# Kernel optimization log

Hardware: AMD Instinct MI355X
Metric: run time of the kernel (lower is better)

The kernel has to match this reference:

```python
import jax, jax.numpy as jnp
import numpy as np

# --- problem sizes (fixed channel widths come from the module's irreps arithmetic) ---
N, E = 100000, 1600000
NUM_ELEM, F0, RB, HID = 4, 4, 10, 10          # len(atomic_list), embedding_dim[0], embedding_dim[1], hidden_dim
EDGE_DIM, SH_DIM = 2 * F0 + RB, 9             # 18, lmax=2 -> 1+3+5
GATE_IN, GATE_OUT = 92, 76                    # 12 scalars + 16 gates + 64 gated ; 12 + 64
CUTOFF, P_ENV, AVG_DEG = 5.0, 6, 16.0


def setup_inputs() -> dict:
    key = jax.random.key(0)
    ks = jax.random.split(key, 16)
    d = {}
    d["type_indices"] = jax.random.randint(ks[0], (N,), 0, NUM_ELEM)
    d["positions"] = jax.random.uniform(ks[1], (N, 3), dtype=jnp.float32) * 6.0
    # radius_graph replaced by a fixed-size random edge list (jit-friendly, same downstream math)
    d["edge_src"] = jax.random.randint(ks[2], (E,), 0, N)
    d["edge_dest"] = jax.random.randint(ks[3], (E,), 0, N)
    d["embed_table"] = jax.random.normal(ks[4], (NUM_ELEM, F0), dtype=jnp.float32)
    fins = [F0, GATE_OUT, GATE_OUT]
    fouts = [GATE_IN, GATE_IN, 1]
    for i in range(3):
        d[f"mlp{i+1}_w1"] = jax.random.normal(ks[5 + 3 * i], (EDGE_DIM, HID), dtype=jnp.float32) / np.float32(np.sqrt(EDGE_DIM))
        d[f"mlp{i+1}_w2"] = jax.random.normal(ks[6 + 3 * i], (HID, SH_DIM), dtype=jnp.float32) / np.float32(np.sqrt(HID))
        d[f"tp{i+1}"] = jax.random.normal(ks[7 + 3 * i], (SH_DIM, fins[i], fouts[i]), dtype=jnp.float32) / np.float32(np.sqrt(fins[i]))
    return d


def sph_harmonics(vec):
    # real spherical harmonics up to l=2, 'component' normalization, on normalized vectors
    r = jnp.linalg.norm(vec, axis=-1, keepdims=True)
    u = vec / jnp.maximum(r, 1e-9)
    x, y, z = u[:, 0], u[:, 1], u[:, 2]
    c1 = np.float32(np.sqrt(3.0))
    c2 = np.float32(np.sqrt(15.0))
    c2b = np.float32(np.sqrt(5.0) / 2.0)
    return jnp.stack([
        jnp.ones_like(x),
        c1 * y, c1 * z, c1 * x,
        c2 * x * y, c2 * y * z, c2b * (3.0 * z * z - 1.0), c2 * x * z, (c2 / 2.0) * (x * x - y * y),
    ], axis=-1)  # [E, 9]


def radial_embed(r):
    # Bessel radial basis with DimeNet-style polynomial envelope (p=6)
    x = r / CUTOFF                                    # [E, 1]
    n = jnp.arange(1, RB + 1, dtype=jnp.float32)      # [RB]
    bess = np.float32(np.sqrt(2.0 / CUTOFF)) * jnp.sin(n * jnp.pi * x) / jnp.maximum(r, 1e-9)
    p = P_ENV
    env = (1.0 - (p + 1) * (p + 2) / 2.0 * x ** p + p * (p + 2) * x ** (p + 1) - p * (p + 1) / 2.0 * x ** (p + 2))
    return bess * env                                 # [E, RB]


def gate(x):
    # e3nn Gate: scalars 4x0e(relu)+8x0o(abs), gates 4x0e(relu)+4x0o(tanh)+4x0e(relu)+4x0o(tanh),
    # gated irreps 4x1o+4x1e (3 comps each) + 4x2e+4x2o (5 comps each)
    s, g, v = x[:, :12], x[:, 12:28], x[:, 28:]
    s_act = jnp.concatenate([jax.nn.relu(s[:, :4]), jnp.abs(s[:, 4:])], axis=-1)
    g_act = jnp.concatenate([jax.nn.relu(g[:, 0:4]), jnp.tanh(g[:, 4:8]),
                             jax.nn.relu(g[:, 8:12]), jnp.tanh(g[:, 12:16])], axis=-1)
    g_exp = jnp.concatenate([jnp.repeat(g_act[:, :8], 3, axis=1),   # 8 gates x 3 comps (l=1)
                             jnp.repeat(g_act[:, 8:], 5, axis=1)],  # 8 gates x 5 comps (l=2)
                            axis=-1)                                 # [*, 64]
    return jnp.concatenate([s_act, v * g_exp], axis=-1)             # [*, 76]


def conv(x, edge_src, edge_dest, sh, edge_embed, w1, w2, tp):
    # per-edge weights from 2-layer MLP on edge embedding, one weight per SH component (factorized TP)
    w = jax.nn.relu(edge_embed @ w1) @ w2             # [E, 9]
    shw = sh * w                                      # [E, 9]
    xg = x[edge_src]                                  # gather [E, F_in]
    msg = shw[:, 0:1] * (xg @ tp[0])
    for s in range(1, SH_DIM):                        # fixed small loop over SH components
        msg = msg + shw[:, s:s + 1] * (xg @ tp[s])
    out = jax.ops.segment_sum(msg, edge_dest, num_segments=x.shape[0])
    return out / np.float32(np.sqrt(AVG_DEG))


def reference(type_indices, positions, edge_src, edge_dest, embed_table,
              mlp1_w1, mlp1_w2, tp1, mlp2_w1, mlp2_w2, tp2, mlp3_w1, mlp3_w2, tp3):
    te = embed_table[type_indices]                            # [N, 4]
    ev = positions[edge_dest] - positions[edge_src]           # [E, 3]
    el = jnp.linalg.norm(ev, axis=-1, keepdims=True)          # [E, 1]
    ee = jnp.concatenate([te[edge_dest], te[edge_src], radial_embed(el)], axis=-1)  # [E, 18]
    sh = sph_harmonics(ev)                                    # [E, 9]
    x0 = te
    x1 = gate(conv(x0, edge_src, edge_dest, sh, ee, mlp1_w1, mlp1_w2, tp1))
    x1 = x1.at[:, :F0].add(x0)                                # scalar-channel residual
    x2 = gate(conv(x1, edge_src, edge_dest, sh, ee, mlp2_w1, mlp2_w2, tp2)) + x1
    x3 = conv(x2, edge_src, edge_dest, sh, ee, mlp3_w1, mlp3_w2, tp3)  # [N, 1]
    return jnp.sum(x3)
```

## Files before the change

kernel.cpp:

```cpp
#include <hip/hip_runtime.h>
#include <hip/hip_bf16.h>
#include <math.h>

typedef unsigned int uint32;
typedef __attribute__((ext_vector_type(8))) short short8;
typedef __attribute__((ext_vector_type(4))) float f32x4;

#define TBINS 1024
#define RMAX  10.4f
#define BSHIFT 7
#define BDR    (1<<BSHIFT)

__device__ __forceinline__ uint32 pack_bf16(float a, float b){
  __hip_bfloat16 ba = __float2bfloat16(a);
  __hip_bfloat16 bb = __float2bfloat16(b);
  unsigned short ua = *reinterpret_cast<unsigned short*>(&ba);
  unsigned short ub = *reinterpret_cast<unsigned short*>(&bb);
  return (uint32)ua | ((uint32)ub << 16);
}
__device__ __forceinline__ float bf_lo(uint32 u){ return __uint_as_float(u << 16); }
__device__ __forceinline__ float bf_hi(uint32 u){ return __uint_as_float(u & 0xffff0000u); }


__global__ __launch_bounds__(1024) void k_bcount(
    const int* __restrict__ esrc, const int* __restrict__ edst,
    int* __restrict__ gb1, int* __restrict__ gb2, int E){
  __shared__ int c1[1024], c2[1024];
  int tid = threadIdx.x;
  c1[tid] = 0; c2[tid] = 0;
  __syncthreads();
  int e0 = blockIdx.x * 8192;
  #pragma unroll
  for (int k=0;k<8;k++){
    int e = e0 + k*1024 + tid;
    if (e < E){
      atomicAdd(&c1[edst[e] >> BSHIFT], 1);
      atomicAdd(&c2[esrc[e] >> BSHIFT], 1);
    }
  }
  __syncthreads();
  if (c1[tid]) atomicAdd(&gb1[tid], c1[tid]);
  if (c2[tid]) atomicAdd(&gb2[tid], c2[tid]);
}


__global__ __launch_bounds__(1024) void k_bscan(
    const int* __restrict__ gb1, const int* __restrict__ gb2,
    int* __restrict__ boff1, int* __restrict__ boff2,
    int* __restrict__ gcur1, int* __restrict__ gcur2,
    int* __restrict__ offsets, int* __restrict__ off2,
    int N, int E, int NBUCK){
  __shared__ int sm[1024];
  int tid = threadIdx.x;
  int v = (tid < NBUCK) ? gb1[tid] : 0;
  sm[tid] = v; __syncthreads();
  for (int off=1; off<1024; off<<=1){
    int t = (tid >= off) ? sm[tid-off] : 0;
    __syncthreads();
    sm[tid] += t;
    __syncthreads();
  }
  if (tid < NBUCK){ int o = sm[tid]-v; boff1[tid] = o; gcur1[tid] = o; }
  __syncthreads();
  int v2 = (tid < NBUCK) ? gb2[tid] : 0;
  sm[tid] = v2; __syncthreads();
  for (int off=1; off<1024; off<<=1){
    int t = (tid >= off) ? sm[tid-off] : 0;
    __syncthreads();
    sm[tid] += t;
    __syncthreads();
  }
  if (tid < NBUCK){ int o = sm[tid]-v2; boff2[tid] = o; gcur2[tid] = o; }
  if (tid == 0){
    boff1[NBUCK] = E; boff2[NBUCK] = E;
    offsets[N] = E;   off2[N] = E;
  }
}


__global__ __launch_bounds__(1024) void k_binA2(
    const int* __restrict__ esrc, const int* __restrict__ edst,
    int* __restrict__ gcur1, int* __restrict__ gcur2,
    int2* __restrict__ pair1, int2* __restrict__ pair2, int E, int NBUCK){
  __shared__ int cnt1[1024], run1[1024];
  __shared__ int cnt2[1024], run2[1024];
  int tid = threadIdx.x;
  int e0 = blockIdx.x * 8192;
  cnt1[tid] = 0; cnt2[tid] = 0;
  __syncthreads();
  #pragma unroll
  for (int k=0;k<8;k++){
    int e = e0 + k*1024 + tid;
    if (e < E){
      atomicAdd(&cnt1[edst[e] >> BSHIFT], 1);
      atomicAdd(&cnt2[esrc[e] >> BSHIFT], 1);
    }
  }
  __syncthreads();
  if (tid < NBUCK){
    if (cnt1[tid] > 0) run1[tid] = atomicAdd(&gcur1[tid], cnt1[tid]);
    if (cnt2[tid] > 0) run2[tid] = atomicAdd(&gcur2[tid], cnt2[tid]);
  }
  __syncthreads();
  #pragma unroll
  for (int k=0;k<8;k++){
    int e = e0 + k*1024 + tid;
    if (e < E){
      int s = esrc[e], d = edst[e];
      int p1 = atomicAdd(&run1[d >> BSHIFT], 1);
      int2 pr1; pr1.x = s; pr1.y = d;
      pair1[p1] = pr1;
      int p2 = atomicAdd(&run2[s >> BSHIFT], 1);
      int2 pr2; pr2.x = d; pr2.y = s;
      pair2[p2] = pr2;
    }
  }
}


__global__ __launch_bounds__(256) void k_binB2(
    const int2* __restrict__ pair, const int* __restrict__ boff,
    int* __restrict__ offsets, int* __restrict__ csr_out, int N){
  __shared__ int cnt[BDR];
  __shared__ int scn[BDR];
  int base = blockIdx.x << BSHIFT;
  int hi = base + BDR; if (hi > N) hi = N;
  int nloc = hi - base;
  if (nloc <= 0) return;
  int tid = threadIdx.x;
  if (tid < BDR) cnt[tid] = 0;
  __syncthreads();
  int p0 = boff[blockIdx.x], p1 = boff[blockIdx.x+1];
  for (int p = p0 + tid; p < p1; p += 256) atomicAdd(&cnt[pair[p].y - base], 1);
  __syncthreads();
  int val = (tid < BDR) ? cnt[tid] : 0;
  if (tid < BDR) scn[tid] = val;
  __syncthreads();
  for (int off=1; off<BDR; off<<=1){
    int t = (tid >= off && tid < BDR) ? scn[tid-off] : 0;
    __syncthreads();
    if (tid < BDR) scn[tid] += t;
    __syncthreads();
  }
  if (tid < nloc){
    int o = p0 + scn[tid] - val;
    offsets[base + tid] = o;
    cnt[tid] = o;
  }
  __syncthreads();
  for (int p = p0 + tid; p < p1; p += 256){
    int2 pr = pair[p];
    int slot = atomicAdd(&cnt[pr.y - base], 1);
    csr_out[slot] = pr.x;
  }
}


__global__ void k_pack(const float* __restrict__ pos, const int* __restrict__ types,
                       float4* __restrict__ ptyp, int N){
  int i = blockIdx.x*256 + threadIdx.x;
  if (i >= N) return;
  float4 f; f.x = pos[3*i]; f.y = pos[3*i+1]; f.z = pos[3*i+2]; f.w = __int_as_float(types[i]);
  ptyp[i] = f;
}


__device__ __forceinline__ void radial_mlp(
    float r, int td, int ts, const float* sEmb,
    const float* sW1, const float* sW2, float* w_out ){
  float ee[18];
  #pragma unroll
  for (int i=0;i<4;i++){ ee[i] = sEmb[td*4+i]; ee[4+i] = sEmb[ts*4+i]; }
  float rm = fmaxf(r, 1e-9f);
  float inv = 1.f/rm;
  float xx = r * 0.2f;
  float x2v = xx*xx, x3v = x2v*xx, x6 = x3v*x3v, x7 = x6*xx, x8 = x7*xx;
  float env = 1.f - 28.f*x6 + 48.f*x7 - 21.f*x8;
  const float bc = 0.6324555320336759f;
  float pref = bc * env * inv;
  const float PI = 3.14159265358979323846f;
  float s1, cth;
  __sincosf(PI*xx, &s1, &cth);
  float two_c = 2.f*cth;
  float sp = 0.f, sc = s1;
  ee[8] = pref * sc;
  #pragma unroll
  for (int n=2;n<=10;n++){
    float sn = two_c*sc - sp;
    sp = sc; sc = sn;
    ee[7+n] = pref * sc;
  }
  float h[10];
  #pragma unroll
  for (int j=0;j<10;j++){
    float a = 0.f;
    #pragma unroll
    for (int k=0;k<18;k++) a = fmaf(ee[k], sW1[k*10+j], a);
    h[j] = fmaxf(a, 0.f);
  }
  #pragma unroll
  for (int sj=0;sj<9;sj++){
    float a = 0.f;
    #pragma unroll
    for (int j=0;j<10;j++) a = fmaf(h[j], sW2[j*9+sj], a);
    w_out[sj] = a;
  }
}


__global__ __launch_bounds__(256) void k_mktab(
    const float* __restrict__ embed,
    const float* __restrict__ w1a, const float* __restrict__ w2a,
    const float* __restrict__ w1b, const float* __restrict__ w2b,
    const float* __restrict__ w1c, const float* __restrict__ w2c,
    uint32* __restrict__ tab){
  __shared__ float sEmb[16];
  __shared__ float sW1a[180], sW2a[90], sW1b[180], sW2b[90], sW1c[180], sW2c[90];
  int t = threadIdx.x;
  if (t < 16) sEmb[t] = embed[t];
  if (t < 180){ sW1a[t] = w1a[t]; sW1b[t] = w1b[t]; sW1c[t] = w1c[t]; }
  if (t < 90){  sW2a[t] = w2a[t]; sW2b[t] = w2b[t]; sW2c[t] = w2c[t]; }
  __syncthreads();
  int gid = blockIdx.x*256 + t;
  if (gid >= 16*TBINS) return;
  int combo = gid / TBINS, bin = gid - combo*TBINS;
  int td = combo >> 2, ts = combo & 3;
  const float dR = RMAX / TBINS;
  float r0 = bin*dR, r1 = r0 + dR;
  float a0[9], a1[9], b0[9], b1[9], c0[9], c1[9];
  radial_mlp(r0, td, ts, sEmb, sW1a, sW2a, a0);
  radial_mlp(r1, td, ts, sEmb, sW1a, sW2a, a1);
  radial_mlp(r0, td, ts, sEmb, sW1b, sW2b, b0);
  radial_mlp(r1, td, ts, sEmb, sW1b, sW2b, b1);
  radial_mlp(r0, td, ts, sEmb, sW1c, sW2c, c0);
  radial_mlp(r1, td, ts, sEmb, sW1c, sW2c, c1);
  uint32* rec = tab + (size_t)gid*32;
  #pragma unroll
  for (int s=0;s<9;s++){
    rec[s]    = pack_bf16(a0[s], a1[s]-a0[s]);
    rec[9+s]  = pack_bf16(b0[s], b1[s]-b0[s]);
    rec[18+s] = pack_bf16(c0[s], c1[s]-c0[s]);
  }
  #pragma unroll
  for (int s=27;s<32;s++) rec[s] = 0u;
}


__global__ __launch_bounds__(256) void k_layer12t(
    const int* __restrict__ offsets, const int* __restrict__ csr_src,
    const float4* __restrict__ ptyp, const float* __restrict__ embed,
    const uint32* __restrict__ tab, const float* __restrict__ tp1,
    float* __restrict__ x1, uint32* __restrict__ shwb, int N, int E){
  __shared__ float sT[36*92];
  __shared__ float sEmb[16];
  int t = threadIdx.x;
  if (t < 16) sEmb[t] = embed[t];
  for (int i=t; i<36*92; i+=256) sT[i] = tp1[i]*0.25f;
  __syncthreads();
  int gid = blockIdx.x*256 + t;
  int n = gid >> 2, q = gid & 3;
  if (n >= N) return;
  float4 fd = ptyp[n];
  float dx = fd.x, dy = fd.y, dz = fd.z;
  int td = __float_as_int(fd.w);
  const float c1 = 1.7320508075688772f, c2 = 3.872983346207417f, c2b = 1.118033988749895f;
  const float invD = (float)TBINS / RMAX;
  float Z[36];
  #pragma unroll
  for (int i=0;i<36;i++) Z[i]=0.f;
  int b0 = offsets[n], b1 = offsets[n+1];
  for (int j=b0+q; j<b1; j+=4){
    int s = csr_src[j];
    float4 fs = ptyp[s];
    float px = dx - fs.x, py = dy - fs.y, pz = dz - fs.z;
    int ts_ = __float_as_int(fs.w);
    float r = sqrtf(px*px + py*py + pz*pz);
    float inv = 1.f/fmaxf(r, 1e-9f);
    float ux = px*inv, uy = py*inv, uz = pz*inv;
    float sh[9];
    sh[0]=1.f; sh[1]=c1*uy; sh[2]=c1*uz; sh[3]=c1*ux;
    sh[4]=c2*ux*uy; sh[5]=c2*uy*uz; sh[6]=c2b*(3.f*uz*uz-1.f); sh[7]=c2*ux*uz;
    sh[8]=0.5f*c2*(ux*ux-uy*uy);
    float tt = r * invD;
    int bb = (int)tt; bb = (bb > TBINS-1) ? TBINS-1 : bb;
    float frac = tt - (float)bb;
    const uint32* rec = tab + ((size_t)((td*4+ts_)*TBINS + bb))*32;
    uint32 R[20];
    #pragma unroll
    for (int i=0;i<5;i++) *(uint4*)&R[i*4] = *(const uint4*)(rec + i*4);
    float x0[4];
    #pragma unroll
    for (int i=0;i<4;i++) x0[i] = sEmb[ts_*4+i];
    float sw2[9];
    #pragma unroll
    for (int sj=0;sj<9;sj++){
      uint32 ua = R[sj], ub = R[9+sj];
      float w1v = fmaf(frac, bf_hi(ua), bf_lo(ua));
      float w2v = fmaf(frac, bf_hi(ub), bf_lo(ub));
      float s1v = sh[sj]*w1v;
      sw2[sj] = sh[sj]*w2v;
      #pragma unroll
      for (int i=0;i<4;i++) Z[sj*4+i] = fmaf(s1v, x0[i], Z[sj*4+i]);
    }
    shwb[j]             = pack_bf16(sw2[0],sw2[1]);
    shwb[(size_t)E+j]   = pack_bf16(sw2[2],sw2[3]);
    shwb[(size_t)2*E+j] = pack_bf16(sw2[4],sw2[5]);
    shwb[(size_t)3*E+j] = pack_bf16(sw2[6],sw2[7]);
    shwb[(size_t)4*E+j] = pack_bf16(sw2[8],0.f);
  }
  #pragma unroll
  for (int m=1; m<=2; m<<=1){
    #pragma unroll
    for (int i=0;i<36;i++) Z[i] += __shfl_xor(Z[i], m, 4);
  }
  float* xo = x1 + (size_t)n*76;
  int gi_prev = -1; float ga = 0.f;
  for (int cc=q*19; cc<q*19+19; cc++){
    float v;
    if (cc < 12){
      float y = 0.f;
      #pragma unroll
      for (int p=0;p<36;p++) y = fmaf(Z[p], sT[p*92+cc], y);
      v = (cc<4) ? (fmaxf(y,0.f) + sEmb[td*4+cc]) : fabsf(y);
    } else {
      int j = cc - 12;
      int gi = (j<24) ? (j/3) : (8 + (j-24)/5);
      if (gi != gi_prev){
        float gy = 0.f;
        #pragma unroll
        for (int p=0;p<36;p++) gy = fmaf(Z[p], sT[p*92+12+gi], gy);
        ga = (gi<4 || (gi>=8 && gi<12)) ? fmaxf(gy,0.f) : tanhf(gy);
        gi_prev = gi;
      }
      float y = 0.f;
      #pragma unroll
      for (int p=0;p<36;p++) y = fmaf(Z[p], sT[p*92+28+j], y);
      v = y*ga;
    }
    xo[cc] = v;
  }
}


__global__ void k_cast(const float* __restrict__ x1, uint32* __restrict__ x1b, int n38){
  int i = blockIdx.x*256 + threadIdx.x;
  if (i >= n38) return;
  float2 f = *(const float2*)&x1[(size_t)i*2];
  x1b[i] = pack_bf16(f.x, f.y);
}


__global__ __launch_bounds__(256) void k_conv2c(
    const int* __restrict__ offsets, const int* __restrict__ csr_src,
    const uint32* __restrict__ shwb, const uint32* __restrict__ x1b,
    uint32* __restrict__ Z2u, int d0, int dend, int E){
  int g = blockIdx.x*256 + threadIdx.x;
  int dg = g/38;
  int u = g - dg*38;
  int d = d0 + dg;
  if (d >= dend) return;
  float z[9], zb[9];
  #pragma unroll
  for (int s=0;s<9;s++){ z[s]=0.f; zb[s]=0.f; }
  int b0 = offsets[d], b1 = offsets[d+1];
  for (int j=b0;j<b1;j++){
    int sn = csr_src[j];
    uint32 xv = x1b[(size_t)sn*38 + u];
    float xa = bf_lo(xv), xb = bf_hi(xv);
    uint32 a0 = shwb[j];
    uint32 a1 = shwb[(size_t)E+j];
    uint32 a2 = shwb[(size_t)2*E+j];
    uint32 a3 = shwb[(size_t)3*E+j];
    uint32 a4 = shwb[(size_t)4*E+j];
    float w[9];
    w[0]=bf_lo(a0); w[1]=bf_hi(a0); w[2]=bf_lo(a1); w[3]=bf_hi(a1);
    w[4]=bf_lo(a2); w[5]=bf_hi(a2); w[6]=bf_lo(a3); w[7]=bf_hi(a3); w[8]=bf_lo(a4);
    #pragma unroll
    for (int s=0;s<9;s++){
      z[s]  = fmaf(w[s], xa, z[s]);
      zb[s] = fmaf(w[s], xb, zb[s]);
    }
  }
  uint32* zr = Z2u + (size_t)dg*352;
  #pragma unroll
  for (int s=0;s<9;s++) zr[s*38+u] = pack_bf16(z[s], zb[s]);
  if (u < 10) zr[342+u] = 0u;
}


__global__ void k_wprep2(const float* __restrict__ tp2, unsigned short* __restrict__ Wt){
  int q = blockIdx.x*256 + threadIdx.x;
  if (q >= 22*96*32) return;
  int kin = q & 31;
  int rest = q >> 5;
  int col = rest % 96, s = rest / 96;
  int k = s*32 + kin;
  float v = (k < 684 && col < 92) ? tp2[k*92+col]*0.25f : 0.f;
  __hip_bfloat16 b = __float2bfloat16(v);
  Wt[q] = *reinterpret_cast<unsigned short*>(&b);
}


__global__ __launch_bounds__(256) void k_gemm2m(
    const uint32* __restrict__ Z2u, const unsigned short* __restrict__ Wt,
    const float* __restrict__ x1, const float* __restrict__ tp3,
    float* __restrict__ A, int d0, int dend){
  __shared__ float lw[64][100];
  __shared__ float tl3[684];
  int t = threadIdx.x;
  for (int i=t;i<684;i+=256) tl3[i] = tp3[i]*0.25f;
  int w = t >> 6, l = t & 63;
  int lrow = l & 15, lk = l >> 4;
  int mb = blockIdx.x*64;
  const uint32* arow = Z2u + (size_t)(mb + w*16 + lrow)*352 + lk*4;
  const short8* bb = (const short8*)Wt;
  int boff = lrow*4 + lk;
  f32x4 acc[6];
  #pragma unroll
  for (int ct=0;ct<6;ct++) acc[ct] = (f32x4){0.f,0.f,0.f,0.f};
  for (int s=0;s<22;s++){
    short8 af = *(const short8*)(arow + s*16);
    #pragma unroll
    for (int ct=0;ct<6;ct++){
      short8 bf = bb[(s*96 + ct*16)*4 + boff];
      acc[ct] = __builtin_amdgcn_mfma_f32_16x16x32_bf16(af, bf, acc[ct], 0, 0, 0);
    }
  }
  #pragma unroll
  for (int ct=0;ct<6;ct++)
    #pragma unroll
    for (int i=0;i<4;i++)
      lw[w*16 + lk*4 + i][ct*16 + lrow] = acc[ct][i];
  __syncthreads();
  int m = t>>2, q = t&3;
  int node = d0 + mb + m;
  float pA[9];
  #pragma unroll
  for (int s=0;s<9;s++) pA[s]=0.f;
  if (node < dend){
    const float* xr = x1 + (size_t)node*76;
    for (int cc=q*19; cc<q*19+19; cc++){
      float v;
      if (cc < 12){
        float y = lw[m][cc];
        v = (cc<4) ? fmaxf(y,0.f) : fabsf(y);
      } else {
        int j = cc-12;
        int gi = (j<24) ? (j/3) : (8 + (j-24)/5);
        float gy = lw[m][12+gi];
        float ga = (gi<4 || (gi>=8 && gi<12)) ? fmaxf(gy,0.f) : tanhf(gy);
        v = lw[m][28+j]*ga;
      }
      float xv = v + xr[cc];
      #pragma unroll
      for (int s=0;s<9;s++) pA[s] = fmaf(xv, tl3[s*76+cc], pA[s]);
    }
  }
  #pragma unroll
  for (int off=1; off<=2; off<<=1){
    #pragma unroll
    for (int s=0;s<9;s++) pA[s] += __shfl_xor(pA[s], off, 4);
  }
  if (node < dend && q == 0){
    float* Ar = A + (size_t)node*16;
    float4 w0 = {pA[0],pA[1],pA[2],pA[3]};
    float4 w1 = {pA[4],pA[5],pA[6],pA[7]};
    *(float4*)Ar = w0;
    *(float4*)(Ar+4) = w1;
    Ar[8] = pA[8];
  }
}


__global__ __launch_bounds__(256) void k_g3t(
    const int* __restrict__ off2, const int* __restrict__ csr2_dst,
    const float4* __restrict__ ptyp, const uint32* __restrict__ tab,
    float* __restrict__ G, int N){
  int gid = blockIdx.x*256 + threadIdx.x;
  int n = gid >> 2, q = gid & 3;
  if (n >= N) return;
  float acc[9];
  #pragma unroll
  for (int s=0;s<9;s++) acc[s]=0.f;
  float4 fs = ptyp[n];
  float sx = fs.x, sy = fs.y, sz = fs.z;
  int ts_ = __float_as_int(fs.w);
  const float c1 = 1.7320508075688772f, c2 = 3.872983346207417f, c2b = 1.118033988749895f;
  const float invD = (float)TBINS / RMAX;
  int b0 = off2[n], b1 = off2[n+1];
  for (int j=b0+q; j<b1; j+=4){
    int d = csr2_dst[j];
    float4 fdd = ptyp[d];
    float px = fdd.x-sx, py = fdd.y-sy, pz = fdd.z-sz;
    int td_ = __float_as_int(fdd.w);
    float r = sqrtf(px*px + py*py + pz*pz);
    float inv = 1.f/fmaxf(r, 1e-9f);
    float ux = px*inv, uy = py*inv, uz = pz*inv;
    float sh[9];
    sh[0]=1.f; sh[1]=c1*uy; sh[2]=c1*uz; sh[3]=c1*ux;
    sh[4]=c2*ux*uy; sh[5]=c2*uy*uz; sh[6]=c2b*(3.f*uz*uz-1.f); sh[7]=c2*ux*uz;
    sh[8]=0.5f*c2*(ux*ux-uy*uy);
    float tt = r * invD;
    int bb = (int)tt; bb = (bb > TBINS-1) ? TBINS-1 : bb;
    float frac = tt - (float)bb;
    const uint32* rec = tab + ((size_t)((td_*4+ts_)*TBINS + bb))*32;
    uint32 R[12];
    #pragma unroll
    for (int i=0;i<3;i++) *(uint4*)&R[i*4] = *(const uint4*)(rec + 16 + i*4);
    #pragma unroll
    for (int sj=0;sj<9;sj++){
      uint32 u = R[2+sj];
      float w = fmaf(frac, bf_hi(u), bf_lo(u));
      acc[sj] = fmaf(sh[sj], w, acc[sj]);
    }
  }
  #pragma unroll
  for (int off=2; off>0; off>>=1){
    #pragma unroll
    for (int s=0;s<9;s++) acc[s] += __shfl_down(acc[s], off, 4);
  }
  if (q == 0){
    float* gr = G + (size_t)n*12;
    float4 w0 = {acc[0],acc[1],acc[2],acc[3]};
    float4 w1 = {acc[4],acc[5],acc[6],acc[7]};
    *(float4*)gr = w0;
    *(float4*)(gr+4) = w1;
    gr[8] = acc[8];
  }
}


__global__ __launch_bounds__(256) void k_finalG(
    const float* __restrict__ G, const float* __restrict__ A,
    float* __restrict__ out, int N){
  int n = blockIdx.x*256 + threadIdx.x;
  float part = 0.f;
  if (n < N){
    const float* gr = G + (size_t)n*12;
    const float* Ar = A + (size_t)n*16;
    float4 g0 = *(const float4*)gr, g1 = *(const float4*)(gr+4);
    float4 a0 = *(const float4*)Ar, a1 = *(const float4*)(Ar+4);
    part = g0.x*a0.x + g0.y*a0.y + g0.z*a0.z + g0.w*a0.w
         + g1.x*a1.x + g1.y*a1.y + g1.z*a1.z + g1.w*a1.w
         + gr[8]*Ar[8];
  }
  #pragma unroll
  for (int off=32; off>0; off>>=1) part += __shfl_down(part, off, 64);
  if ((threadIdx.x & 63) == 0) atomicAdd(out, part);
}


extern "C" void kernel_launch(void* const* d_in, const int* in_sizes, int n_in,
                              void* d_out, int out_size, void* d_ws, size_t ws_size,
                              hipStream_t stream){
  const int*   types = (const int*)d_in[0];
  const float* pos   = (const float*)d_in[1];
  const int*   esrc  = (const int*)d_in[2];
  const int*   edst  = (const int*)d_in[3];
  const float* embed = (const float*)d_in[4];
  const float* m1w1=(const float*)d_in[5],  *m1w2=(const float*)d_in[6],  *tp1=(const float*)d_in[7];
  const float* m2w1=(const float*)d_in[8],  *m2w2=(const float*)d_in[9],  *tp2=(const float*)d_in[10];
  const float* m3w1=(const float*)d_in[11], *m3w2=(const float*)d_in[12], *tp3=(const float*)d_in[13];
  int N = in_sizes[0];
  int E = in_sizes[2];
  float* out = (float*)d_out;

  char* wsb = (char*)d_ws; size_t off = 0;
  auto alloc = [&](size_t b)->char*{ char* p = wsb + off; off = (off + b + 255) & ~(size_t)255; return p; };
  float*  x1      = (float*)alloc((size_t)N*76*sizeof(float));
  uint32* x1b     = (uint32*)alloc((size_t)N*38*sizeof(uint32));
  float4* ptyp    = (float4*)alloc((size_t)N*sizeof(float4));
  uint32* shwb    = (uint32*)alloc((size_t)E*5*sizeof(uint32));
  int*    csr_src = (int*)alloc((size_t)E*sizeof(int));
  int*    csr2_dst= (int*)alloc((size_t)E*sizeof(int));
  int2*   pair1   = (int2*)alloc((size_t)E*sizeof(int2));
  int2*   pair2   = (int2*)alloc((size_t)E*sizeof(int2));
  int*    offsets = (int*)alloc((size_t)(N+1)*sizeof(int));
  int*    off2    = (int*)alloc((size_t)(N+1)*sizeof(int));
  int*    gb1     = (int*)alloc(1024*sizeof(int));
  int*    gb2     = (int*)alloc(1024*sizeof(int));
  int*    boff1   = (int*)alloc(1025*sizeof(int));
  int*    boff2   = (int*)alloc(1025*sizeof(int));
  int*    gcur1   = (int*)alloc(1024*sizeof(int));
  int*    gcur2   = (int*)alloc(1024*sizeof(int));
  unsigned short* Wt = (unsigned short*)alloc((size_t)22*96*32*sizeof(unsigned short));
  float*  A       = (float*)alloc((size_t)N*16*sizeof(float));
  float*  G       = (float*)alloc((size_t)N*12*sizeof(float));
  uint32* tab     = (uint32*)alloc((size_t)16*TBINS*32*sizeof(uint32));

  size_t avail = (ws_size > off) ? (ws_size - off - 512) : 0;
  long long rows = (long long)(avail / (352*sizeof(uint32))) - 64;
  int CH = (rows > 50176) ? 50176 : (int)rows;
  CH = (CH / 64) * 64;
  if (CH < 64) CH = 64;
  uint32* Z2u = (uint32*)alloc((size_t)(CH+64)*352*sizeof(uint32));

  hipMemsetAsync(gb1, 0, 2048*sizeof(int), stream);
  hipMemsetAsync(out, 0, sizeof(float), stream);

  int nbN = (N+255)/256;
  int nbT = (16*TBINS+255)/256;
  int NBUCK = (N + BDR - 1) >> BSHIFT;
  int nbC = (E+8191)/8192;
  k_pack<<<nbN,256,0,stream>>>(pos, types, ptyp, N);
  k_mktab<<<nbT,256,0,stream>>>(embed, m1w1, m1w2, m2w1, m2w2, m3w1, m3w2, tab);
  k_bcount<<<nbC,1024,0,stream>>>(esrc, edst, gb1, gb2, E);
  k_bscan<<<1,1024,0,stream>>>(gb1, gb2, boff1, boff2, gcur1, gcur2,
                               offsets, off2, N, E, NBUCK);
  k_binA2<<<nbC,1024,0,stream>>>(esrc, edst, gcur1, gcur2, pair1, pair2, E, NBUCK);
  k_binB2<<<NBUCK,256,0,stream>>>(pair1, boff1, offsets, csr_src, N);
  k_binB2<<<NBUCK,256,0,stream>>>(pair2, boff2, off2, csr2_dst, N);

  k_wprep2<<<(22*96*32+255)/256,256,0,stream>>>(tp2, Wt);

  k_g3t<<<(4*N+255)/256,256,0,stream>>>(off2, csr2_dst, ptyp, tab, G, N);

  k_layer12t<<<(4*N+255)/256,256,0,stream>>>(offsets, csr_src, ptyp, embed,
                                             tab, tp1, x1, shwb, N, E);
  k_cast<<<(N*38+255)/256,256,0,stream>>>(x1, x1b, N*38);

  for (int d0 = 0; d0 < N; d0 += CH){
    int dend = (d0 + CH < N) ? (d0 + CH) : N;
    int nn = dend - d0;
    k_conv2c<<<((nn*38)+255)/256,256,0,stream>>>(offsets, csr_src, shwb, x1b, Z2u, d0, dend, E);
    k_gemm2m<<<(nn+63)/64,256,0,stream>>>(Z2u, Wt, x1, tp3, A, d0, dend);
  }

  k_finalG<<<nbN,256,0,stream>>>(G, A, out, N);
}
```

Baseline: 499.4 us.

## Parallelize layer-1 edge work over block edges with LDS atomic accumulation by source type

The layer-1 kernel previously gave each destination node four threads that walked its edges, accumulating a 36-float register array. Each block now covers 64 destination nodes and spreads their contiguous CSR edge range evenly across all 256 threads, using a binary search over local offsets to find each edge's destination. Per-edge results are folded into a per-node, per-source-type 9-wide sum in shared memory with atomics, and the embedding is applied afterwards. This is meant to fix load imbalance from variable node degree and to cut per-edge FMAs, at the cost of LDS atomic contention, the binary search, and an extra synchronization.

```diff
diff --git a/kernel.cpp b/kernel.cpp
--- a/kernel.cpp
+++ b/kernel.cpp
@@ -246,33 +246,37 @@
 }
 
 
-__global__ __launch_bounds__(256) void k_layer12t(
+__global__ __launch_bounds__(256) void k_edgeA2(
     const int* __restrict__ offsets, const int* __restrict__ csr_src,
     const float4* __restrict__ ptyp, const float* __restrict__ embed,
     const uint32* __restrict__ tab, const float* __restrict__ tp1,
     float* __restrict__ x1, uint32* __restrict__ shwb, int N, int E){
   __shared__ float sT[36*92];
   __shared__ float sEmb[16];
+  __shared__ float S[64*36];
+  __shared__ int loff[65];
   int t = threadIdx.x;
+  int n0 = blockIdx.x*64;
+  int nloc = N - n0; if (nloc > 64) nloc = 64;
+  if (nloc <= 0) return;
   if (t < 16) sEmb[t] = embed[t];
   for (int i=t; i<36*92; i+=256) sT[i] = tp1[i]*0.25f;
-  __syncthreads();
-  int gid = blockIdx.x*256 + t;
-  int n = gid >> 2, q = gid & 3;
-  if (n >= N) return;
-  float4 fd = ptyp[n];
-  float dx = fd.x, dy = fd.y, dz = fd.z;
-  int td = __float_as_int(fd.w);
+  for (int i=t; i<64*36; i+=256) S[i] = 0.f;
+  for (int i=t; i<=64; i+=256) loff[i] = offsets[n0 + (i<nloc ? i : nloc)];
+  __syncthreads();
   const float c1 = 1.7320508075688772f, c2 = 3.872983346207417f, c2b = 1.118033988749895f;
   const float invD = (float)TBINS / RMAX;
-  float Z[36];
-  #pragma unroll
-  for (int i=0;i<36;i++) Z[i]=0.f;
-  int b0 = offsets[n], b1 = offsets[n+1];
-  for (int j=b0+q; j<b1; j+=4){
+  int p0 = loff[0], p1 = loff[64];
+  for (int j = p0 + t; j < p1; j += 256){
+    int lo = 0, hi = 64;
+    #pragma unroll
+    for (int it=0; it<6; it++){ int mid = (lo+hi)>>1; if (loff[mid] <= j) lo = mid; else hi = mid; }
+    int d = lo;
+    float4 fd = ptyp[n0+d];
+    int td = __float_as_int(fd.w);
     int s = csr_src[j];
     float4 fs = ptyp[s];
-    float px = dx - fs.x, py = dy - fs.y, pz = dz - fs.z;
+    float px = fd.x - fs.x, py = fd.y - fs.y, pz = fd.z - fs.z;
     int ts_ = __float_as_int(fs.w);
     float r = sqrtf(px*px + py*py + pz*pz);
     float inv = 1.f/fmaxf(r, 1e-9f);
@@ -288,19 +292,15 @@
     uint32 R[20];
     #pragma unroll
     for (int i=0;i<5;i++) *(uint4*)&R[i*4] = *(const uint4*)(rec + i*4);
-    float x0[4];
-    #pragma unroll
-    for (int i=0;i<4;i++) x0[i] = sEmb[ts_*4+i];
+    float* Sd = &S[d*36 + ts_*9];
     float sw2[9];
     #pragma unroll
     for (int sj=0;sj<9;sj++){
       uint32 ua = R[sj], ub = R[9+sj];
       float w1v = fmaf(frac, bf_hi(ua), bf_lo(ua));
       float w2v = fmaf(frac, bf_hi(ub), bf_lo(ub));
-      float s1v = sh[sj]*w1v;
       sw2[sj] = sh[sj]*w2v;
-      #pragma unroll
-      for (int i=0;i<4;i++) Z[sj*4+i] = fmaf(s1v, x0[i], Z[sj*4+i]);
+      atomicAdd(&Sd[sj], sh[sj]*w1v);
     }
     shwb[j]             = pack_bf16(sw2[0],sw2[1]);
     shwb[(size_t)E+j]   = pack_bf16(sw2[2],sw2[3]);
@@ -308,11 +308,22 @@
     shwb[(size_t)3*E+j] = pack_bf16(sw2[6],sw2[7]);
     shwb[(size_t)4*E+j] = pack_bf16(sw2[8],0.f);
   }
-  #pragma unroll
-  for (int m=1; m<=2; m<<=1){
-    #pragma unroll
-    for (int i=0;i<36;i++) Z[i] += __shfl_xor(Z[i], m, 4);
-  }
+  __syncthreads();
+  int d = t >> 2, q = t & 3;
+  if (d >= nloc) return;
+  int n = n0 + d;
+  int td = __float_as_int(ptyp[n].w);
+  float Z[36];
+  const float* Sd = &S[d*36];
+  #pragma unroll
+  for (int sj=0;sj<9;sj++)
+    #pragma unroll
+    for (int i=0;i<4;i++){
+      float z = 0.f;
+      #pragma unroll
+      for (int t4=0;t4<4;t4++) z = fmaf(sEmb[t4*4+i], Sd[t4*9+sj], z);
+      Z[sj*4+i] = z;
+    }
   float* xo = x1 + (size_t)n*76;
   int gi_prev = -1; float ga = 0.f;
   for (int cc=q*19; cc<q*19+19; cc++){
@@ -599,6 +610,7 @@
   hipMemsetAsync(out, 0, sizeof(float), stream);
 
   int nbN = (N+255)/256;
+  int nbB = (N+63)/64;
   int nbT = (16*TBINS+255)/256;
   int NBUCK = (N + BDR - 1) >> BSHIFT;
   int nbC = (E+8191)/8192;
@@ -615,8 +627,8 @@
 
   k_g3t<<<(4*N+255)/256,256,0,stream>>>(off2, csr2_dst, ptyp, tab, G, N);
 
-  k_layer12t<<<(4*N+255)/256,256,0,stream>>>(offsets, csr_src, ptyp, embed,
-                                             tab, tp1, x1, shwb, N, E);
+  k_edgeA2<<<nbB,256,0,stream>>>(offsets, csr_src, ptyp, embed, tab, tp1,
+                                 x1, shwb, N, E);
   k_cast<<<(N*38+255)/256,256,0,stream>>>(x1, x1b, N*38);
 
   for (int d0 = 0; d0 < N; d0 += CH){
```

Result: slower. 554.6 us (+11.1%).

## Fuse layer-2 edge aggregation and MFMA GEMM into one kernel via LDS

Applied to the files above, without the earlier changes.

Merges the chunked conv2 aggregation kernel and the MFMA GEMM/gate kernel into one kernel. Each block now aggregates 32 destination nodes into an LDS tile and runs the bf16 MFMA GEMM from LDS instead of from a global Z2 buffer. This removes the global write and re-read of the large intermediate and the chunked launch loop. In exchange, blocks are smaller, use more LDS, and leave half the threads idle in the epilogue. The per-block gather phase can also be imbalanced across nodes of different degree.

```diff
diff --git a/kernel.cpp b/kernel.cpp
--- a/kernel.cpp
+++ b/kernel.cpp
@@ -350,44 +350,6 @@
 }
 
 
-__global__ __launch_bounds__(256) void k_conv2c(
-    const int* __restrict__ offsets, const int* __restrict__ csr_src,
-    const uint32* __restrict__ shwb, const uint32* __restrict__ x1b,
-    uint32* __restrict__ Z2u, int d0, int dend, int E){
-  int g = blockIdx.x*256 + threadIdx.x;
-  int dg = g/38;
-  int u = g - dg*38;
-  int d = d0 + dg;
-  if (d >= dend) return;
-  float z[9], zb[9];
-  #pragma unroll
-  for (int s=0;s<9;s++){ z[s]=0.f; zb[s]=0.f; }
-  int b0 = offsets[d], b1 = offsets[d+1];
-  for (int j=b0;j<b1;j++){
-    int sn = csr_src[j];
-    uint32 xv = x1b[(size_t)sn*38 + u];
-    float xa = bf_lo(xv), xb = bf_hi(xv);
-    uint32 a0 = shwb[j];
-    uint32 a1 = shwb[(size_t)E+j];
-    uint32 a2 = shwb[(size_t)2*E+j];
-    uint32 a3 = shwb[(size_t)3*E+j];
-    uint32 a4 = shwb[(size_t)4*E+j];
-    float w[9];
-    w[0]=bf_lo(a0); w[1]=bf_hi(a0); w[2]=bf_lo(a1); w[3]=bf_hi(a1);
-    w[4]=bf_lo(a2); w[5]=bf_hi(a2); w[6]=bf_lo(a3); w[7]=bf_hi(a3); w[8]=bf_lo(a4);
-    #pragma unroll
-    for (int s=0;s<9;s++){
-      z[s]  = fmaf(w[s], xa, z[s]);
-      zb[s] = fmaf(w[s], xb, zb[s]);
-    }
-  }
-  uint32* zr = Z2u + (size_t)dg*352;
-  #pragma unroll
-  for (int s=0;s<9;s++) zr[s*38+u] = pack_bf16(z[s], zb[s]);
-  if (u < 10) zr[342+u] = 0u;
-}
-
-
 __global__ void k_wprep2(const float* __restrict__ tp2, unsigned short* __restrict__ Wt){
   int q = blockIdx.x*256 + threadIdx.x;
   if (q >= 22*96*32) return;
@@ -401,43 +363,87 @@
 }
 
 
-__global__ __launch_bounds__(256) void k_gemm2m(
-    const uint32* __restrict__ Z2u, const unsigned short* __restrict__ Wt,
-    const float* __restrict__ x1, const float* __restrict__ tp3,
-    float* __restrict__ A, int d0, int dend){
-  __shared__ float lw[64][100];
+__global__ __launch_bounds__(256) void k_conv2gemm(
+    const int* __restrict__ offsets, const int* __restrict__ csr_src,
+    const uint32* __restrict__ shwb, const uint32* __restrict__ x1b,
+    const unsigned short* __restrict__ Wt, const float* __restrict__ x1,
+    const float* __restrict__ tp3, float* __restrict__ A, int N, int E){
+  __shared__ __align__(16) uint32 Zl[32*356];
+  __shared__ float lw[32][100];
   __shared__ float tl3[684];
   int t = threadIdx.x;
+  int n0 = blockIdx.x*32;
+  int nloc = N - n0; if (nloc > 32) nloc = 32;
+  if (nloc <= 0) return;
   for (int i=t;i<684;i+=256) tl3[i] = tp3[i]*0.25f;
+  __syncthreads();
+  for (int p = t; p < nloc*38; p += 256){
+    int dg = p/38;
+    int u = p - dg*38;
+    int d = n0 + dg;
+    float z[9], zb[9];
+    #pragma unroll
+    for (int s=0;s<9;s++){ z[s]=0.f; zb[s]=0.f; }
+    int b0 = offsets[d], b1 = offsets[d+1];
+    for (int j=b0;j<b1;j++){
+      int sn = csr_src[j];
+      uint32 xv = x1b[(size_t)sn*38 + u];
+      float xa = bf_lo(xv), xb = bf_hi(xv);
+      uint32 a0 = shwb[j];
+      uint32 a1 = shwb[(size_t)E+j];
+      uint32 a2 = shwb[(size_t)2*E+j];
+      uint32 a3 = shwb[(size_t)3*E+j];
+      uint32 a4 = shwb[(size_t)4*E+j];
+      float w[9];
+      w[0]=bf_lo(a0); w[1]=bf_hi(a0); w[2]=bf_lo(a1); w[3]=bf_hi(a1);
+      w[4]=bf_lo(a2); w[5]=bf_hi(a2); w[6]=bf_lo(a3); w[7]=bf_hi(a3); w[8]=bf_lo(a4);
+      #pragma unroll
+      for (int s=0;s<9;s++){
+        z[s]  = fmaf(w[s], xa, z[s]);
+        zb[s] = fmaf(w[s], xb, zb[s]);
+      }
+    }
+    uint32* zr = &Zl[dg*356];
+    #pragma unroll
+    for (int s=0;s<9;s++) zr[s*38+u] = pack_bf16(z[s], zb[s]);
+    if (u < 10) zr[342+u] = 0u;
+  }
+  for (int i = nloc*356 + t; i < 32*356; i += 256) Zl[i] = 0u;
+  __syncthreads();
   int w = t >> 6, l = t & 63;
+  int h = w & 1, chg = w >> 1;
   int lrow = l & 15, lk = l >> 4;
-  int mb = blockIdx.x*64;
-  const uint32* arow = Z2u + (size_t)(mb + w*16 + lrow)*352 + lk*4;
+  const uint32* arow = &Zl[(h*16 + lrow)*356 + lk*4];
   const short8* bb = (const short8*)Wt;
   int boff = lrow*4 + lk;
-  f32x4 acc[6];
-  #pragma unroll
-  for (int ct=0;ct<6;ct++) acc[ct] = (f32x4){0.f,0.f,0.f,0.f};
+  f32x4 acc[3];
+  #pragma unroll
+  for (int ct=0;ct<3;ct++) acc[ct] = (f32x4){0.f,0.f,0.f,0.f};
   for (int s=0;s<22;s++){
     short8 af = *(const short8*)(arow + s*16);
     #pragma unroll
-    for (int ct=0;ct<6;ct++){
-      short8 bf = bb[(s*96 + ct*16)*4 + boff];
+    for (int ct=0;ct<3;ct++){
+      int ctg = chg*3 + ct;
+      short8 bf = bb[(s*96 + ctg*16)*4 + boff];
       acc[ct] = __builtin_amdgcn_mfma_f32_16x16x32_bf16(af, bf, acc[ct], 0, 0, 0);
     }
   }
-  #pragma unroll
-  for (int ct=0;ct<6;ct++)
+  __syncthreads();
+  #pragma unroll
+  for (int ct=0;ct<3;ct++){
+    int ctg = chg*3 + ct;
     #pragma unroll
     for (int i=0;i<4;i++)
-      lw[w*16 + lk*4 + i][ct*16 + lrow] = acc[ct][i];
+      lw[h*16 + lk*4 + i][ctg*16 + lrow] = acc[ct][i];
+  }
   __syncthreads();
   int m = t>>2, q = t&3;
-  int node = d0 + mb + m;
   float pA[9];
   #pragma unroll
   for (int s=0;s<9;s++) pA[s]=0.f;
-  if (node < dend){
+  int node = n0 + m;
+  bool act = (m < nloc) && (t < 128);
+  if (act){
     const float* xr = x1 + (size_t)node*76;
     for (int cc=q*19; cc<q*19+19; cc++){
       float v;
@@ -461,7 +467,7 @@
     #pragma unroll
     for (int s=0;s<9;s++) pA[s] += __shfl_xor(pA[s], off, 4);
   }
-  if (node < dend && q == 0){
+  if (act && q == 0){
     float* Ar = A + (size_t)node*16;
     float4 w0 = {pA[0],pA[1],pA[2],pA[3]};
     float4 w1 = {pA[4],pA[5],pA[6],pA[7]};
@@ -588,13 +594,6 @@
   float*  G       = (float*)alloc((size_t)N*12*sizeof(float));
   uint32* tab     = (uint32*)alloc((size_t)16*TBINS*32*sizeof(uint32));
 
-  size_t avail = (ws_size > off) ? (ws_size - off - 512) : 0;
-  long long rows = (long long)(avail / (352*sizeof(uint32))) - 64;
-  int CH = (rows > 50176) ? 50176 : (int)rows;
-  CH = (CH / 64) * 64;
-  if (CH < 64) CH = 64;
-  uint32* Z2u = (uint32*)alloc((size_t)(CH+64)*352*sizeof(uint32));
-
   hipMemsetAsync(gb1, 0, 2048*sizeof(int), stream);
   hipMemsetAsync(out, 0, sizeof(float), stream);
 
@@ -619,12 +618,8 @@
                                              tab, tp1, x1, shwb, N, E);
   k_cast<<<(N*38+255)/256,256,0,stream>>>(x1, x1b, N*38);
 
-  for (int d0 = 0; d0 < N; d0 += CH){
-    int dend = (d0 + CH < N) ? (d0 + CH) : N;
-    int nn = dend - d0;
-    k_conv2c<<<((nn*38)+255)/256,256,0,stream>>>(offsets, csr_src, shwb, x1b, Z2u, d0, dend, E);
-    k_gemm2m<<<(nn+63)/64,256,0,stream>>>(Z2u, Wt, x1, tp3, A, d0, dend);
-  }
+  k_conv2gemm<<<(N+31)/32,256,0,stream>>>(offsets, csr_src, shwb, x1b,
+                                          Wt, x1, tp3, A, N, E);
 
   k_finalG<<<nbN,256,0,stream>>>(G, A, out, N);
 }
```

After: 744.9 us. 1.49x slower.
